# Kernel optimization log

Measured on AMD Instinct MI355X. Metric: run time of the kernel, lower is better.

The kernel has to match this reference:

```python
import jax, jax.numpy as jnp
import numpy as np

B, S, D_IN, HEAD_DIM = 4, 4096, 1024, 128

def setup_inputs() -> dict:
    key = jax.random.key(0)
    k1, k2, k3, k4 = jax.random.split(key, 4)
    x = jax.random.normal(k1, (B, S, D_IN), dtype=jnp.float32)
    # nn.Parameter(torch.rand(...)) -> uniform [0,1)
    W_query = jax.random.uniform(k2, (D_IN, HEAD_DIM), dtype=jnp.float32)
    W_key = jax.random.uniform(k3, (D_IN, HEAD_DIM), dtype=jnp.float32)
    W_value = jax.random.uniform(k4, (D_IN, HEAD_DIM), dtype=jnp.float32)
    return {"x": x, "W_query": W_query, "W_key": W_key, "W_value": W_value}

def reference(x, W_query, W_key, W_value):
    # x: [B,S,d_in]; W_*: [d_in,head_dim]
    queries = jnp.einsum('bsd,dh->bsh', x, W_query)
    keys = jnp.einsum('bsd,dh->bsh', x, W_key)
    values = jnp.einsum('bsd,dh->bsh', x, W_value)
    scale = 1.0 / jnp.sqrt(jnp.asarray(HEAD_DIM, dtype=x.dtype))
    attn_scores = jnp.einsum('bqh,bkh->bqk', queries, keys)  # [B,S,S]
    attn_weights = jax.nn.softmax(attn_scores * scale, axis=-1)
    context_vec = jnp.einsum('bqk,bkh->bqh', attn_weights, values)
    return context_vec
```

## Files before the change

kernel.cpp:

```cpp
#include <hip/hip_runtime.h>
#include <cstdint>

#define B_  4
#define S_  4096
#define DIN 1024
#define DH  128
#define QSCALE (0.08838834764831845f * 1.4426950408889634f)

typedef short bf16x8 __attribute__((ext_vector_type(8)));
typedef float f32x4 __attribute__((ext_vector_type(4)));
typedef unsigned short u16;
typedef unsigned int   u32;

#define MFMA16(a, b, c) __builtin_amdgcn_mfma_f32_16x16x32_bf16(a, b, c, 0, 0, 0)

#define GLOAD_LDS16(g, l) __builtin_amdgcn_global_load_lds( \
    (const __attribute__((address_space(1))) void*)(g),     \
    (__attribute__((address_space(3))) void*)(l), 16, 0, 0)

#if __has_builtin(__builtin_amdgcn_exp2f)
#define EXP2(x) __builtin_amdgcn_exp2f(x)
#else
#define EXP2(x) exp2f(x)
#endif

__device__ inline u16 bf16_rn(float f) {
    union { float f; u32 u; } v; v.f = f;
    u32 r = v.u + 0x7FFFu + ((v.u >> 16) & 1u);
    return (u16)(r >> 16);
}
__device__ inline float bf16_f(u16 h) {
    union { u32 u; float f; } v; v.u = ((u32)h) << 16; return v.f;
}
__device__ inline u32 pk2(float a, float b) {
    return (u32)bf16_rn(a) | ((u32)bf16_rn(b) << 16);
}
__device__ inline void split2(float a, float b, u32& hi, u32& lo) {
    u32 ua = __builtin_bit_cast(u32, a), ub = __builtin_bit_cast(u32, b);
    u32 ha = ua & 0xFFFF0000u, hb = ub & 0xFFFF0000u;
    hi = (ua >> 16) | hb;
    float la = a - __builtin_bit_cast(float, ha);
    float lb = b - __builtin_bit_cast(float, hb);
    lo = (u32)bf16_rn(la) | ((u32)bf16_rn(lb) << 16);
}

__global__ __launch_bounds__(256) void wconv2(
    const float* __restrict__ Wq, const float* __restrict__ Wk, const float* __restrict__ Wv,
    u16* __restrict__ wpack)
{
    int id  = blockIdx.x * 256 + threadIdx.x;
    int s   = id / 2560;
    int rem = id % 2560;
    int p   = rem >> 9;
    int gi  = rem & 511;
    int n   = gi & 127, kq2 = gi >> 7;
    const float* W = (p < 2) ? Wq : (p < 4) ? Wk : Wv;
    int k0 = 32 * s + 8 * kq2;
    u16 o[8];
    #pragma unroll
    for (int j = 0; j < 8; ++j) {
        float v = W[(size_t)(k0 + j) * DH + n];
        if (p < 2) v *= QSCALE;
        if (p == 4) {
            o[j] = bf16_rn(v);
        } else {
            u32 u = __builtin_bit_cast(u32, v);
            if ((p & 1) == 0) o[j] = (u16)(u >> 16);
            else o[j] = bf16_rn(v - __builtin_bit_cast(float, u & 0xFFFF0000u));
        }
    }
    u16* dst = wpack + (size_t)id * 8;
    *(uint4*)dst = *(uint4*)o;
}

__global__ __launch_bounds__(512) void qkv_v8(
    const float* __restrict__ x, const u16* __restrict__ wpack,
    u16* __restrict__ qhi, u16* __restrict__ qlo,
    u16* __restrict__ khi, u16* __restrict__ klo, u16* __restrict__ vt)
{
    __shared__ __align__(16) char lds[81920];

    const int t    = threadIdx.x;
    const int row0 = blockIdx.x * 64;
    const int lane = t & 63, wave = t >> 6;
    const int l15  = lane & 15, g = lane >> 4;
    const int wr   = wave >> 1;
    const int wc   = wave & 1;

    f32x4 accq[4], acck[4], accv[4];
    #pragma unroll
    for (int nt = 0; nt < 4; ++nt)
        #pragma unroll
        for (int r = 0; r < 4; ++r) {
            accq[nt][r] = 0.f; acck[nt][r] = 0.f; accv[nt][r] = 0.f;
        }

    const char* WP = (const char*)wpack;
    auto stage = [&](int bufi, int s) {
        char* d = lds + bufi * 40960;
        const char* src = WP + (size_t)s * 40960;
        #pragma unroll
        for (int c = 0; c < 5; ++c) {
            int o = t * 16 + c * 8192;
            GLOAD_LDS16(src + o, d + o);
        }
    };

    const float* xp = x + (size_t)(row0 + 16 * wr + l15) * DIN + 8 * g;

    float4 ca = *(const float4*)(xp);
    float4 cb = *(const float4*)(xp + 4);

    stage(0, 0);
    __syncthreads();

    int buf = 0;
    for (int s = 0; s < 32; ++s) {
        if (s < 31) stage(buf ^ 1, s + 1);

        float4 na, nb;
        if (s < 31) {
            na = *(const float4*)(xp + 32 * (s + 1));
            nb = *(const float4*)(xp + 32 * (s + 1) + 4);
        }

        bf16x8 xh, xl;
        {
            uint4 H, L;
            split2(ca.x, ca.y, H.x, L.x); split2(ca.z, ca.w, H.y, L.y);
            split2(cb.x, cb.y, H.z, L.z); split2(cb.z, cb.w, H.w, L.w);
            xh = __builtin_bit_cast(bf16x8, H);
            xl = __builtin_bit_cast(bf16x8, L);
        }

        const char* wb = lds + buf * 40960;
        #pragma unroll
        for (int nt = 0; nt < 4; ++nt) {
            const int n  = 64 * wc + 16 * nt + l15;
            const int wo = (g << 11) + (n << 4);
            bf16x8 qwh = *(const bf16x8*)(wb + wo);
            bf16x8 qwl = *(const bf16x8*)(wb +  8192 + wo);
            bf16x8 kwh = *(const bf16x8*)(wb + 16384 + wo);
            bf16x8 kwl = *(const bf16x8*)(wb + 24576 + wo);
            bf16x8 vwh = *(const bf16x8*)(wb + 32768 + wo);
            accq[nt] = MFMA16(xh, qwh, accq[nt]);
            accq[nt] = MFMA16(xl, qwh, accq[nt]);
            accq[nt] = MFMA16(xh, qwl, accq[nt]);
            acck[nt] = MFMA16(xh, kwh, acck[nt]);
            acck[nt] = MFMA16(xl, kwh, acck[nt]);
            acck[nt] = MFMA16(xh, kwl, acck[nt]);
            accv[nt] = MFMA16(xh, vwh, accv[nt]);
        }
        __syncthreads();
        if (s < 31) { ca = na; cb = nb; }
        buf ^= 1;
    }

    const int bb = row0 >> 12, kt = (row0 & 4095) >> 6;

    #pragma unroll
    for (int reg = 0; reg < 4; ++reg) {
        int r = row0 + 16 * wr + 4 * g + reg;
        #pragma unroll
        for (int nt = 0; nt < 4; ++nt) {
            int c = 64 * wc + 16 * nt + l15;
            float v = accq[nt][reg];
            u32 u = __builtin_bit_cast(u32, v);
            float lo = v - __builtin_bit_cast(float, u & 0xFFFF0000u);
            size_t o = (size_t)r * DH + c;
            qhi[o] = (u16)(u >> 16);
            qlo[o] = bf16_rn(lo);
        }
    }

    u16* lk = (u16*)lds;
    #pragma unroll
    for (int reg = 0; reg < 4; ++reg) {
        int kr = 16 * wr + 4 * g + reg;
        #pragma unroll
        for (int nt = 0; nt < 4; ++nt) {
            int c = 64 * wc + 16 * nt + l15;
            int o = kr * 128 + (((c >> 3) ^ (kr & 15)) << 3) + (c & 7);
            float v = acck[nt][reg];
            u32 u = __builtin_bit_cast(u32, v);
            lk[o]        = (u16)(u >> 16);
            lk[8192 + o] = bf16_rn(v - __builtin_bit_cast(float, u & 0xFFFF0000u));
        }
    }
    __syncthreads();
    {
        char* gk = (char*)(khi + (size_t)(bb * 64 + kt) * 8192);
        char* gl = (char*)(klo + (size_t)(bb * 64 + kt) * 8192);
        #pragma unroll
        for (int c2 = 0; c2 < 2; ++c2) {
            int o = t * 16 + c2 * 8192;
            *(uint4*)(gk + o) = *(const uint4*)(lds + o);
            *(uint4*)(gl + o) = *(const uint4*)(lds + 16384 + o);
        }
    }
    __syncthreads();

    #pragma unroll
    for (int reg = 0; reg < 4; ++reg) {
        int kr = 16 * wr + 4 * g + reg;
        #pragma unroll
        for (int nt = 0; nt < 4; ++nt) {
            int c = 64 * wc + 16 * nt + l15;
            int o = c * 64 + (((kr >> 3) ^ (c & 7)) << 3) + (kr & 7);
            lk[o] = bf16_rn(accv[nt][reg]);
        }
    }
    __syncthreads();
    {
        char* gv = (char*)(vt + (size_t)(bb * 64 + kt) * 8192);
        #pragma unroll
        for (int c2 = 0; c2 < 2; ++c2) {
            int o = t * 16 + c2 * 8192;
            *(uint4*)(gv + o) = *(const uint4*)(lds + o);
        }
    }
}

__global__ __launch_bounds__(512, 2) void flash_db(
    const u16* __restrict__ qhi, const u16* __restrict__ qlo,
    const u16* __restrict__ khi, const u16* __restrict__ klo,
    const u16* __restrict__ vt,
    u16* __restrict__ opart, float2* __restrict__ ml)
{
    __shared__ __align__(16) char smem[2 * 49152];

    const int tid  = threadIdx.x;
    const int wave = tid >> 6, lane = tid & 63;
    const int l15  = lane & 15, g = lane >> 4;
    const int bid  = blockIdx.x;
    const int pair = bid & 15, qt = bid >> 4;
    const int b = pair >> 2, z = pair & 3;

    const int q0row = b * S_ + qt * 256 + wave * 32;

    bf16x8 qh[2][4], ql[2][4];
    #pragma unroll
    for (int h = 0; h < 2; ++h)
        #pragma unroll
        for (int ks = 0; ks < 4; ++ks) {
            size_t qa = (size_t)(q0row + 16 * h + l15) * DH + 32 * ks + 8 * g;
            qh[h][ks] = *(const bf16x8*)(qhi + qa);
            ql[h][ks] = *(const bf16x8*)(qlo + qa);
        }

    f32x4 O0[8], O1[8];
    #pragma unroll
    for (int dt = 0; dt < 8; ++dt)
        #pragma unroll
        for (int r = 0; r < 4; ++r) { O0[dt][r] = 0.f; O1[dt][r] = 0.f; }

    float m0 = -3.0e38f, l0 = 0.f, m1 = -3.0e38f, l1 = 0.f;

    int koff[4];
    #pragma unroll
    for (int ks = 0; ks < 4; ++ks)
        koff[ks] = (((4 * ks + g) ^ l15) << 4) + (l15 << 8);
    int voff[2];
    #pragma unroll
    for (int kw = 0; kw < 2; ++kw)
        voff[kw] = (((4 * kw + g) ^ (l15 & 7)) << 4);

    const char* kbase = (const char*)(khi + (size_t)b * 64 * 8192);
    const char* lbase = (const char*)(klo + (size_t)b * 64 * 8192);
    const char* vbase = (const char*)(vt  + (size_t)b * 64 * 8192);
    const int kt0 = z * 16;

    auto stage = [&](int bufi, int ktl) {
        const char* sk = kbase + (size_t)(kt0 + ktl) * 16384;
        const char* sl = lbase + (size_t)(kt0 + ktl) * 16384;
        const char* sv = vbase + (size_t)(kt0 + ktl) * 16384;
        char* dk = smem + bufi * 49152;
        #pragma unroll
        for (int c = 0; c < 2; ++c) {
            int o = tid * 16 + c * 8192;
            GLOAD_LDS16(sk + o, dk + o);
            GLOAD_LDS16(sl + o, dk + 16384 + o);
            GLOAD_LDS16(sv + o, dk + 32768 + o);
        }
    };

    stage(0, 0);
    __syncthreads();

    int buf = 0;
    for (int ktl = 0; ktl < 16; ++ktl) {
        if (ktl < 15) stage(buf ^ 1, ktl + 1);

        const char* bk = smem + buf * 49152;
        const char* bl = bk + 16384;
        const char* bv = bk + 32768;

        f32x4 s0[4], s1[4];
        #pragma unroll
        for (int nt = 0; nt < 4; ++nt)
            #pragma unroll
            for (int r = 0; r < 4; ++r) { s0[nt][r] = 0.f; s1[nt][r] = 0.f; }

        #pragma unroll
        for (int ks = 0; ks < 4; ++ks) {
            #pragma unroll
            for (int nt = 0; nt < 4; ++nt) {
                bf16x8 kh = *(const bf16x8*)(bk + nt * 4096 + koff[ks]);
                bf16x8 kl = *(const bf16x8*)(bl + nt * 4096 + koff[ks]);
                s0[nt] = MFMA16(kh, qh[0][ks], s0[nt]);
                s0[nt] = MFMA16(kh, ql[0][ks], s0[nt]);
                s0[nt] = MFMA16(kl, qh[0][ks], s0[nt]);
                s1[nt] = MFMA16(kh, qh[1][ks], s1[nt]);
                s1[nt] = MFMA16(kh, ql[1][ks], s1[nt]);
                s1[nt] = MFMA16(kl, qh[1][ks], s1[nt]);
            }
        }

        float ml0 = -3.0e38f, ml1 = -3.0e38f;
        #pragma unroll
        for (int nt = 0; nt < 4; ++nt)
            #pragma unroll
            for (int r = 0; r < 4; ++r) {
                ml0 = fmaxf(ml0, s0[nt][r]);
                ml1 = fmaxf(ml1, s1[nt][r]);
            }
        ml0 = fmaxf(ml0, __shfl_xor(ml0, 16));
        ml0 = fmaxf(ml0, __shfl_xor(ml0, 32));
        ml1 = fmaxf(ml1, __shfl_xor(ml1, 16));
        ml1 = fmaxf(ml1, __shfl_xor(ml1, 32));

        if (!__all((ml0 <= m0 + 8.0f) & (ml1 <= m1 + 8.0f))) {
            float mn0 = fmaxf(m0, ml0), mn1 = fmaxf(m1, ml1);
            float fsc0 = EXP2(m0 - mn0), fsc1 = EXP2(m1 - mn1);
            m0 = mn0; m1 = mn1;
            l0 *= fsc0; l1 *= fsc1;
            float fr0[4], fr1[4];
            #pragma unroll
            for (int r = 0; r < 4; ++r) {
                fr0[r] = __shfl(fsc0, 4 * g + r);
                fr1[r] = __shfl(fsc1, 4 * g + r);
            }
            #pragma unroll
            for (int dt = 0; dt < 8; ++dt)
                #pragma unroll
                for (int r = 0; r < 4; ++r) {
                    O0[dt][r] *= fr0[r];
                    O1[dt][r] *= fr1[r];
                }
        }

        u32 pk0[4][2], pk1[4][2];
        float ps0 = 0.f, ps1 = 0.f;
        #pragma unroll
        for (int nt = 0; nt < 4; ++nt) {
            float a0 = EXP2(s0[nt][0] - m0), a1 = EXP2(s0[nt][1] - m0);
            float a2 = EXP2(s0[nt][2] - m0), a3 = EXP2(s0[nt][3] - m0);
            ps0 += (a0 + a1) + (a2 + a3);
            pk0[nt][0] = pk2(a0, a1);
            pk0[nt][1] = pk2(a2, a3);
            float c0 = EXP2(s1[nt][0] - m1), c1 = EXP2(s1[nt][1] - m1);
            float c2 = EXP2(s1[nt][2] - m1), c3 = EXP2(s1[nt][3] - m1);
            ps1 += (c0 + c1) + (c2 + c3);
            pk1[nt][0] = pk2(c0, c1);
            pk1[nt][1] = pk2(c2, c3);
        }
        ps0 += __shfl_xor(ps0, 16);
        ps0 += __shfl_xor(ps0, 32);
        ps1 += __shfl_xor(ps1, 16);
        ps1 += __shfl_xor(ps1, 32);
        l0 += ps0; l1 += ps1;

        const int s0l = l15 | ((2 * (g & 1)) << 4);
        const int s1l = s0l + 16;
        const int hiH = g >> 1;
        #pragma unroll
        for (int kw = 0; kw < 2; ++kw) {
            u32 a0, a1, a2, a3, c0, c1, c2, c3;
            {
                u32 x0 = __shfl(pk0[2 * kw][0], s0l), y0 = __shfl(pk0[2 * kw + 1][0], s0l);
                u32 x1 = __shfl(pk0[2 * kw][1], s0l), y1 = __shfl(pk0[2 * kw + 1][1], s0l);
                u32 x2 = __shfl(pk0[2 * kw][0], s1l), y2 = __shfl(pk0[2 * kw + 1][0], s1l);
                u32 x3 = __shfl(pk0[2 * kw][1], s1l), y3 = __shfl(pk0[2 * kw + 1][1], s1l);
                a0 = hiH ? y0 : x0; a1 = hiH ? y1 : x1;
                a2 = hiH ? y2 : x2; a3 = hiH ? y3 : x3;
            }
            {
                u32 x0 = __shfl(pk1[2 * kw][0], s0l), y0 = __shfl(pk1[2 * kw + 1][0], s0l);
                u32 x1 = __shfl(pk1[2 * kw][1], s0l), y1 = __shfl(pk1[2 * kw + 1][1], s0l);
                u32 x2 = __shfl(pk1[2 * kw][0], s1l), y2 = __shfl(pk1[2 * kw + 1][0], s1l);
                u32 x3 = __shfl(pk1[2 * kw][1], s1l), y3 = __shfl(pk1[2 * kw + 1][1], s1l);
                c0 = hiH ? y0 : x0; c1 = hiH ? y1 : x1;
                c2 = hiH ? y2 : x2; c3 = hiH ? y3 : x3;
            }
            union { u32 w[4]; bf16x8 v; } pa, pb;
            pa.w[0] = a0; pa.w[1] = a1; pa.w[2] = a2; pa.w[3] = a3;
            pb.w[0] = c0; pb.w[1] = c1; pb.w[2] = c2; pb.w[3] = c3;
            #pragma unroll
            for (int dt = 0; dt < 8; ++dt) {
                bf16x8 vf = *(const bf16x8*)(bv + (16 * dt + l15) * 128 + voff[kw]);
                O0[dt] = MFMA16(pa.v, vf, O0[dt]);
                O1[dt] = MFMA16(pb.v, vf, O1[dt]);
            }
        }

        __syncthreads();
        buf ^= 1;
    }

    u16* op = opart + ((size_t)z * 16384 + q0row) * DH;
    #pragma unroll
    for (int dt = 0; dt < 8; ++dt)
        #pragma unroll
        for (int r = 0; r < 4; ++r) {
            op[(size_t)(4 * g + r) * DH + 16 * dt + l15]      = bf16_rn(O0[dt][r]);
            op[(size_t)(16 + 4 * g + r) * DH + 16 * dt + l15] = bf16_rn(O1[dt][r]);
        }
    if (lane < 16) {
        ml[(size_t)z * 16384 + q0row + lane]      = make_float2(m0, l0);
        ml[(size_t)z * 16384 + q0row + 16 + lane] = make_float2(m1, l1);
    }
}

__global__ __launch_bounds__(256) void merge4(
    const u16* __restrict__ op, const float2* __restrict__ ml, float* __restrict__ O)
{
    int row = blockIdx.x * 16 + (threadIdx.x >> 4);
    int dq  = (threadIdx.x & 15) * 8;
    float2 a[4];
    #pragma unroll
    for (int zz = 0; zz < 4; ++zz) a[zz] = ml[(size_t)zz * 16384 + row];
    float M = fmaxf(fmaxf(a[0].x, a[1].x), fmaxf(a[2].x, a[3].x));
    float w[4], den = 0.f;
    #pragma unroll
    for (int zz = 0; zz < 4; ++zz) {
        w[zz] = EXP2(a[zz].x - M);
        den += a[zz].y * w[zz];
    }
    float inv = 1.0f / den;
    float acc[8];
    #pragma unroll
    for (int j = 0; j < 8; ++j) acc[j] = 0.f;
    #pragma unroll
    for (int zz = 0; zz < 4; ++zz) {
        const u16* p = op + ((size_t)zz * 16384 + row) * DH + dq;
        bf16x8 vv = *(const bf16x8*)p;
        #pragma unroll
        for (int j = 0; j < 8; ++j) acc[j] += w[zz] * bf16_f((u16)vv[j]);
    }
    float4 oa, ob;
    oa.x = acc[0] * inv; oa.y = acc[1] * inv; oa.z = acc[2] * inv; oa.w = acc[3] * inv;
    ob.x = acc[4] * inv; ob.y = acc[5] * inv; ob.z = acc[6] * inv; ob.w = acc[7] * inv;
    *(float4*)(O + (size_t)row * DH + dq)     = oa;
    *(float4*)(O + (size_t)row * DH + dq + 4) = ob;
}

extern "C" void kernel_launch(void* const* d_in, const int* in_sizes, int n_in,
                              void* d_out, int out_size, void* d_ws, size_t ws_size,
                              hipStream_t stream) {
    const float* x  = (const float*)d_in[0];
    const float* Wq = (const float*)d_in[1];
    const float* Wk = (const float*)d_in[2];
    const float* Wv = (const float*)d_in[3];
    float* out = (float*)d_out;

    const size_t SZ = (size_t)B_ * S_ * DH;
    u16* qhi = (u16*)d_ws;
    u16* qlo = qhi + SZ;
    u16* khi = qlo + SZ;
    u16* klo = khi + SZ;
    u16* vtp = klo + SZ;
    u16* wpk = vtp + SZ;
    u16* opart = wpk + 655360;
    float2* mlp = (float2*)((char*)opart + (size_t)4 * 16384 * DH * 2);

    wconv2<<<320, 256, 0, stream>>>(Wq, Wk, Wv, wpk);
    qkv_v8<<<256, 512, 0, stream>>>(x, wpk, qhi, qlo, khi, klo, vtp);
    flash_db<<<256, 512, 0, stream>>>(qhi, qlo, khi, klo, vtp, opart, mlp);
    merge4<<<1024, 256, 0, stream>>>(opart, mlp, out);
}
```

Measured before the change: 127.9 us.

## Halve per-wave query rows and drop LDS double buffering in flash kernel

```diff
diff --git a/kernel.cpp b/kernel.cpp
--- a/kernel.cpp
+++ b/kernel.cpp
@@ -221,13 +221,13 @@
     }
 }
 
-__global__ __launch_bounds__(512, 2) void flash_db(
+__global__ __launch_bounds__(512, 2) void flash16(
     const u16* __restrict__ qhi, const u16* __restrict__ qlo,
     const u16* __restrict__ khi, const u16* __restrict__ klo,
     const u16* __restrict__ vt,
     u16* __restrict__ opart, float2* __restrict__ ml)
 {
-    __shared__ __align__(16) char smem[2 * 49152];
+    __shared__ __align__(16) char smem[49152];
 
     const int tid  = threadIdx.x;
     const int wave = tid >> 6, lane = tid & 63;
@@ -236,25 +236,23 @@
     const int pair = bid & 15, qt = bid >> 4;
     const int b = pair >> 2, z = pair & 3;
 
-    const int q0row = b * S_ + qt * 256 + wave * 32;
-
-    bf16x8 qh[2][4], ql[2][4];
-    #pragma unroll
-    for (int h = 0; h < 2; ++h)
-        #pragma unroll
-        for (int ks = 0; ks < 4; ++ks) {
-            size_t qa = (size_t)(q0row + 16 * h + l15) * DH + 32 * ks + 8 * g;
-            qh[h][ks] = *(const bf16x8*)(qhi + qa);
-            ql[h][ks] = *(const bf16x8*)(qlo + qa);
-        }
-
-    f32x4 O0[8], O1[8];
+    const int q0row = b * S_ + qt * 128 + wave * 16;
+
+    bf16x8 qh[4], ql[4];
+    #pragma unroll
+    for (int ks = 0; ks < 4; ++ks) {
+        size_t qa = (size_t)(q0row + l15) * DH + 32 * ks + 8 * g;
+        qh[ks] = *(const bf16x8*)(qhi + qa);
+        ql[ks] = *(const bf16x8*)(qlo + qa);
+    }
+
+    f32x4 O0[8];
     #pragma unroll
     for (int dt = 0; dt < 8; ++dt)
         #pragma unroll
-        for (int r = 0; r < 4; ++r) { O0[dt][r] = 0.f; O1[dt][r] = 0.f; }
-
-    float m0 = -3.0e38f, l0 = 0.f, m1 = -3.0e38f, l1 = 0.f;
+        for (int r = 0; r < 4; ++r) O0[dt][r] = 0.f;
+
+    float m0 = -3.0e38f, l0 = 0.f;
 
     int koff[4];
     #pragma unroll
@@ -270,36 +268,32 @@
     const char* vbase = (const char*)(vt  + (size_t)b * 64 * 8192);
     const int kt0 = z * 16;
 
-    auto stage = [&](int bufi, int ktl) {
+    auto stage = [&](int ktl) {
         const char* sk = kbase + (size_t)(kt0 + ktl) * 16384;
         const char* sl = lbase + (size_t)(kt0 + ktl) * 16384;
         const char* sv = vbase + (size_t)(kt0 + ktl) * 16384;
-        char* dk = smem + bufi * 49152;
         #pragma unroll
         for (int c = 0; c < 2; ++c) {
             int o = tid * 16 + c * 8192;
-            GLOAD_LDS16(sk + o, dk + o);
-            GLOAD_LDS16(sl + o, dk + 16384 + o);
-            GLOAD_LDS16(sv + o, dk + 32768 + o);
+            GLOAD_LDS16(sk + o, smem + o);
+            GLOAD_LDS16(sl + o, smem + 16384 + o);
+            GLOAD_LDS16(sv + o, smem + 32768 + o);
         }
     };
 
-    stage(0, 0);
-    __syncthreads();
-
-    int buf = 0;
     for (int ktl = 0; ktl < 16; ++ktl) {
-        if (ktl < 15) stage(buf ^ 1, ktl + 1);
-
-        const char* bk = smem + buf * 49152;
+        stage(ktl);
+        __syncthreads();
+
+        const char* bk = smem;
         const char* bl = bk + 16384;
         const char* bv = bk + 32768;
 
-        f32x4 s0[4], s1[4];
+        f32x4 s0[4];
         #pragma unroll
         for (int nt = 0; nt < 4; ++nt)
             #pragma unroll
-            for (int r = 0; r < 4; ++r) { s0[nt][r] = 0.f; s1[nt][r] = 0.f; }
+            for (int r = 0; r < 4; ++r) s0[nt][r] = 0.f;
 
         #pragma unroll
         for (int ks = 0; ks < 4; ++ks) {
@@ -307,50 +301,36 @@
             for (int nt = 0; nt < 4; ++nt) {
                 bf16x8 kh = *(const bf16x8*)(bk + nt * 4096 + koff[ks]);
                 bf16x8 kl = *(const bf16x8*)(bl + nt * 4096 + koff[ks]);
-                s0[nt] = MFMA16(kh, qh[0][ks], s0[nt]);
-                s0[nt] = MFMA16(kh, ql[0][ks], s0[nt]);
-                s0[nt] = MFMA16(kl, qh[0][ks], s0[nt]);
-                s1[nt] = MFMA16(kh, qh[1][ks], s1[nt]);
-                s1[nt] = MFMA16(kh, ql[1][ks], s1[nt]);
-                s1[nt] = MFMA16(kl, qh[1][ks], s1[nt]);
+                s0[nt] = MFMA16(kh, qh[ks], s0[nt]);
+                s0[nt] = MFMA16(kh, ql[ks], s0[nt]);
+                s0[nt] = MFMA16(kl, qh[ks], s0[nt]);
             }
         }
 
-        float ml0 = -3.0e38f, ml1 = -3.0e38f;
+        float ml0 = -3.0e38f;
         #pragma unroll
         for (int nt = 0; nt < 4; ++nt)
             #pragma unroll
-            for (int r = 0; r < 4; ++r) {
-                ml0 = fmaxf(ml0, s0[nt][r]);
-                ml1 = fmaxf(ml1, s1[nt][r]);
-            }
+            for (int r = 0; r < 4; ++r) ml0 = fmaxf(ml0, s0[nt][r]);
         ml0 = fmaxf(ml0, __shfl_xor(ml0, 16));
         ml0 = fmaxf(ml0, __shfl_xor(ml0, 32));
-        ml1 = fmaxf(ml1, __shfl_xor(ml1, 16));
-        ml1 = fmaxf(ml1, __shfl_xor(ml1, 32));
-
-        if (!__all((ml0 <= m0 + 8.0f) & (ml1 <= m1 + 8.0f))) {
-            float mn0 = fmaxf(m0, ml0), mn1 = fmaxf(m1, ml1);
-            float fsc0 = EXP2(m0 - mn0), fsc1 = EXP2(m1 - mn1);
-            m0 = mn0; m1 = mn1;
-            l0 *= fsc0; l1 *= fsc1;
-            float fr0[4], fr1[4];
-            #pragma unroll
-            for (int r = 0; r < 4; ++r) {
-                fr0[r] = __shfl(fsc0, 4 * g + r);
-                fr1[r] = __shfl(fsc1, 4 * g + r);
-            }
+
+        if (!__all(ml0 <= m0 + 8.0f)) {
+            float mn0 = fmaxf(m0, ml0);
+            float fsc0 = EXP2(m0 - mn0);
+            m0 = mn0;
+            l0 *= fsc0;
+            float fr0[4];
+            #pragma unroll
+            for (int r = 0; r < 4; ++r) fr0[r] = __shfl(fsc0, 4 * g + r);
             #pragma unroll
             for (int dt = 0; dt < 8; ++dt)
                 #pragma unroll
-                for (int r = 0; r < 4; ++r) {
-                    O0[dt][r] *= fr0[r];
-                    O1[dt][r] *= fr1[r];
-                }
-        }
-
-        u32 pk0[4][2], pk1[4][2];
-        float ps0 = 0.f, ps1 = 0.f;
+                for (int r = 0; r < 4; ++r) O0[dt][r] *= fr0[r];
+        }
+
+        u32 pk0[4][2];
+        float ps0 = 0.f;
         #pragma unroll
         for (int nt = 0; nt < 4; ++nt) {
             float a0 = EXP2(s0[nt][0] - m0), a1 = EXP2(s0[nt][1] - m0);
@@ -358,24 +338,17 @@
             ps0 += (a0 + a1) + (a2 + a3);
             pk0[nt][0] = pk2(a0, a1);
             pk0[nt][1] = pk2(a2, a3);
-            float c0 = EXP2(s1[nt][0] - m1), c1 = EXP2(s1[nt][1] - m1);
-            float c2 = EXP2(s1[nt][2] - m1), c3 = EXP2(s1[nt][3] - m1);
-            ps1 += (c0 + c1) + (c2 + c3);
-            pk1[nt][0] = pk2(c0, c1);
-            pk1[nt][1] = pk2(c2, c3);
         }
         ps0 += __shfl_xor(ps0, 16);
         ps0 += __shfl_xor(ps0, 32);
-        ps1 += __shfl_xor(ps1, 16);
-        ps1 += __shfl_xor(ps1, 32);
-        l0 += ps0; l1 += ps1;
+        l0 += ps0;
 
         const int s0l = l15 | ((2 * (g & 1)) << 4);
         const int s1l = s0l + 16;
         const int hiH = g >> 1;
         #pragma unroll
         for (int kw = 0; kw < 2; ++kw) {
-            u32 a0, a1, a2, a3, c0, c1, c2, c3;
+            u32 a0, a1, a2, a3;
             {
                 u32 x0 = __shfl(pk0[2 * kw][0], s0l), y0 = __shfl(pk0[2 * kw + 1][0], s0l);
                 u32 x1 = __shfl(pk0[2 * kw][1], s0l), y1 = __shfl(pk0[2 * kw + 1][1], s0l);
@@ -384,41 +357,26 @@
                 a0 = hiH ? y0 : x0; a1 = hiH ? y1 : x1;
                 a2 = hiH ? y2 : x2; a3 = hiH ? y3 : x3;
             }
-            {
-                u32 x0 = __shfl(pk1[2 * kw][0], s0l), y0 = __shfl(pk1[2 * kw + 1][0], s0l);
-                u32 x1 = __shfl(pk1[2 * kw][1], s0l), y1 = __shfl(pk1[2 * kw + 1][1], s0l);
-                u32 x2 = __shfl(pk1[2 * kw][0], s1l), y2 = __shfl(pk1[2 * kw + 1][0], s1l);
-                u32 x3 = __shfl(pk1[2 * kw][1], s1l), y3 = __shfl(pk1[2 * kw + 1][1], s1l);
-                c0 = hiH ? y0 : x0; c1 = hiH ? y1 : x1;
-                c2 = hiH ? y2 : x2; c3 = hiH ? y3 : x3;
-            }
-            union { u32 w[4]; bf16x8 v; } pa, pb;
+            union { u32 w[4]; bf16x8 v; } pa;
             pa.w[0] = a0; pa.w[1] = a1; pa.w[2] = a2; pa.w[3] = a3;
-            pb.w[0] = c0; pb.w[1] = c1; pb.w[2] = c2; pb.w[3] = c3;
             #pragma unroll
             for (int dt = 0; dt < 8; ++dt) {
                 bf16x8 vf = *(const bf16x8*)(bv + (16 * dt + l15) * 128 + voff[kw]);
                 O0[dt] = MFMA16(pa.v, vf, O0[dt]);
-                O1[dt] = MFMA16(pb.v, vf, O1[dt]);
             }
         }
 
         __syncthreads();
-        buf ^= 1;
     }
 
     u16* op = opart + ((size_t)z * 16384 + q0row) * DH;
     #pragma unroll
     for (int dt = 0; dt < 8; ++dt)
         #pragma unroll
-        for (int r = 0; r < 4; ++r) {
-            op[(size_t)(4 * g + r) * DH + 16 * dt + l15]      = bf16_rn(O0[dt][r]);
-            op[(size_t)(16 + 4 * g + r) * DH + 16 * dt + l15] = bf16_rn(O1[dt][r]);
-        }
-    if (lane < 16) {
-        ml[(size_t)z * 16384 + q0row + lane]      = make_float2(m0, l0);
-        ml[(size_t)z * 16384 + q0row + 16 + lane] = make_float2(m1, l1);
-    }
+        for (int r = 0; r < 4; ++r)
+            op[(size_t)(4 * g + r) * DH + 16 * dt + l15] = bf16_rn(O0[dt][r]);
+    if (lane < 16)
+        ml[(size_t)z * 16384 + q0row + lane] = make_float2(m0, l0);
 }
 
 __global__ __launch_bounds__(256) void merge4(
@@ -475,6 +433,6 @@
 
     wconv2<<<320, 256, 0, stream>>>(Wq, Wk, Wv, wpk);
     qkv_v8<<<256, 512, 0, stream>>>(x, wpk, qhi, qlo, khi, klo, vtp);
-    flash_db<<<256, 512, 0, stream>>>(qhi, qlo, khi, klo, vtp, opart, mlp);
+    flash16<<<512, 512, 0, stream>>>(qhi, qlo, khi, klo, vtp, opart, mlp);
     merge4<<<1024, 256, 0, stream>>>(opart, mlp, out);
 }
```

New measurement: 131.4 us. 1.03x slower.
